# Kernel optimization log

Hardware: AMD Instinct MI355X
Metric: run time of the kernel (lower is better)

Reference implementation:

```python
import jax, jax.numpy as jnp
import numpy as np

WS = 7  # window size

def rel_pos_index(ws):
    coords = np.stack(np.meshgrid(np.arange(ws), np.arange(ws), indexing='ij'))  # [2,ws,ws]
    cf = coords.reshape(2, -1)                      # [2, N]
    rel = (cf[:, :, None] - cf[:, None, :]).transpose(1, 2, 0)  # [N,N,2]
    rel[:, :, 0] += ws - 1
    rel[:, :, 1] += ws - 1
    rel[:, :, 0] *= 2 * ws - 1
    return rel.sum(-1)                              # [N,N] int

REL_IDX = rel_pos_index(WS)

def setup_inputs() -> dict:
    key = jax.random.key(0)
    ks = jax.random.split(key, 7)
    B, nW, H, N, D = 32, 64, 6, WS * WS, 32
    C = H * D
    return {
        "x": jax.random.normal(ks[0], (B * nW, N, C), jnp.float32),
        "q_global": jax.random.normal(ks[1], (B, 1, H, N, D), jnp.float32),
        "w_qkv": jax.random.normal(ks[2], (2 * C, C), jnp.float32) * 0.02,
        "b_qkv": jax.random.normal(ks[3], (2 * C,), jnp.float32) * 0.02,
        "bias_table": jax.random.normal(ks[4], ((2 * WS - 1) ** 2, H), jnp.float32) * 0.02,
        "w_proj": jax.random.normal(ks[5], (C, C), jnp.float32) * 0.02,
        "b_proj": jax.random.normal(ks[6], (C,), jnp.float32) * 0.02,
    }

def reference(x, q_global, w_qkv, b_qkv, bias_table, w_proj, b_proj):
    B_, N, C = x.shape
    B, _, H, _, D = q_global.shape
    scale = D ** -0.5
    # K,V projection: [B_, N, 2C] -> two [B_, H, N, D]
    kv = x @ w_qkv.T + b_qkv
    k, v = jnp.split(kv, 2, axis=-1)
    k = k.reshape(B_, N, H, D).transpose(0, 2, 1, 3)
    v = v.reshape(B_, N, H, D).transpose(0, 2, 1, 3)
    # Global query repeated over windows per image
    rep = B_ // B
    q = jnp.broadcast_to(q_global, (B, rep, H, N, D)).reshape(B_, H, N, D) * scale
    attn = jnp.einsum('bhnd,bhmd->bhnm', q, k)  # [B_, H, N, N]
    bias = bias_table[REL_IDX.reshape(-1)].reshape(N, N, H).transpose(2, 0, 1)  # [H,N,N]
    attn = jax.nn.softmax(attn + bias[None], axis=-1)
    out = jnp.einsum('bhnm,bhmd->bhnd', attn, v).transpose(0, 2, 1, 3).reshape(B_, N, C)
    return out @ w_proj.T + b_proj
```

## Files before the change

kernel.cpp:

```cpp
#include <hip/hip_runtime.h>
#include <hip/hip_bf16.h>

typedef __attribute__((ext_vector_type(8))) short short8;
typedef __attribute__((ext_vector_type(4))) short short4v;
typedef __attribute__((ext_vector_type(4))) float f32x4;
typedef __attribute__((ext_vector_type(4))) unsigned int uint32x4;

#define MFMA16(A,B,C) __builtin_amdgcn_mfma_f32_16x16x32_bf16((A),(B),(C),0,0,0)

static __device__ __forceinline__ unsigned short f2bf(float f) {
  return __builtin_bit_cast(unsigned short, __float2bfloat16(f));
}

__global__ void prep_kernel(const float* __restrict__ qg,
                            const float* __restrict__ wqkv,
                            const float* __restrict__ wproj,
                            const float* __restrict__ btab,
                            unsigned short* __restrict__ wq_c,
                            unsigned short* __restrict__ wp_c,
                            unsigned short* __restrict__ q_bf,
                            float* __restrict__ bias_c)
{
  const int t = blockIdx.x * 256 + threadIdx.x;
  if (t < 32*6*64*32) {
    const int d = t & 31, n = (t >> 5) & 63;
    const int bh = t >> 11;
    const int h = bh % 6, b = bh / 6;
    float v = 0.f;
    if (n < 49) v = qg[((b * 6 + h) * 49 + n) * 32 + d] * 0.17677669529663687f;
    q_bf[t] = f2bf(v);
  }
  if (t < 8*3*6*64*8) {
    const int e = t & 7, l = (t >> 3) & 63;
    const int kb = (t >> 9) % 6, g = (t >> 9) / 6;
    const int ct = g % 3, wv = g / 3;
    const int j = wv * 48 + ct * 16 + (l & 15);
    const int c = kb * 32 + (l >> 4) * 8 + e;
    wq_c[t] = f2bf(wqkv[j * 192 + c]);
  }
  if (t < 2*6*6*64*8) {
    const int e = t & 7, l = (t >> 3) & 63;
    const int kb = (t >> 9) % 6, g = (t >> 9) / 6;
    const int ct = g % 6, cc = g / 6;
    const int cp = cc * 96 + ct * 16 + (l & 15);
    const int c = kb * 32 + (l >> 4) * 8 + e;
    wp_c[t] = f2bf(wproj[cp * 192 + c]);
  }
  if (t < 6*4*64*16) {
    const int i4 = t & 15;
    const int mt = i4 >> 2, r = i4 & 3;
    const int l = (t >> 4) & 63;
    const int nt = (t >> 10) & 3;
    const int h = t >> 12;
    const int m = (l >> 4) * 8 + (mt & 1) * 4 + r + (mt >> 1) * 32;
    const int n = nt * 16 + (l & 15);
    float v;
    if (m >= 49) v = -1e30f;
    else if (n >= 49) v = 0.f;
    else {
      const int ci = n / 7, cj = n % 7, mi = m / 7, mj = m % 7;
      const int idx = (ci - mi + 6) * 13 + (cj - mj + 6);
      v = btab[idx * 6 + h];
    }
    bias_c[t] = v;
  }
}

__global__ __launch_bounds__(512, 4)
void fused_win_attn(const float* __restrict__ x,
                    const float* __restrict__ b_qkv,
                    const float* __restrict__ b_proj,
                    const unsigned short* __restrict__ wq_c,
                    const unsigned short* __restrict__ wp_c,
                    const unsigned short* __restrict__ q_bf,
                    const float* __restrict__ bias_c,
                    float* __restrict__ out)
{
  extern __shared__ unsigned short lds[];
  unsigned short* x_lds  = lds;
  unsigned short* k_lds  = lds + 12800;
  unsigned short* vT_lds = lds + 26624;
  unsigned short* o_lds  = lds + 12800;

  const f32x4 ZERO4 = {0.f, 0.f, 0.f, 0.f};
  const int tid = threadIdx.x;
  const int wv = tid >> 6;
  const int l  = tid & 63;
  const int lr = l & 15;
  const int lq = l >> 4;
  const int w  = blockIdx.x;

  {
    const float* xw = x + (size_t)w * (49 * 192);
    for (int i = tid; i < 2352; i += 512) {
      const float4 v = *reinterpret_cast<const float4*>(xw + i * 4);
      const int e = i * 4;
      const int row = e / 192, col = e % 192;
      short4v pk;
      pk[0] = (short)f2bf(v.x); pk[1] = (short)f2bf(v.y);
      pk[2] = (short)f2bf(v.z); pk[3] = (short)f2bf(v.w);
      *reinterpret_cast<short4v*>(&x_lds[row * 200 + col]) = pk;
    }
    for (int i = tid; i < 720; i += 512) {
      const int e = i * 4;
      const int row = 49 + e / 192, col = e % 192;
      short4v z = {0, 0, 0, 0};
      *reinterpret_cast<short4v*>(&x_lds[row * 200 + col]) = z;
    }
  }
  __syncthreads();

  {
    short8 afr[4][6];
#pragma unroll
    for (int mt = 0; mt < 4; ++mt)
#pragma unroll
      for (int kb = 0; kb < 6; ++kb)
        afr[mt][kb] = *reinterpret_cast<const short8*>(
            &x_lds[(mt * 16 + lr) * 200 + kb * 32 + lq * 8]);

    for (int ct = 0; ct < 3; ++ct) {
      const int j = wv * 48 + ct * 16 + lr;
      short8 bfr[6];
#pragma unroll
      for (int kb = 0; kb < 6; ++kb)
        bfr[kb] = *reinterpret_cast<const short8*>(
            &wq_c[((((wv * 3) + ct) * 6 + kb) * 64 + l) * 8]);
      const float bq = b_qkv[j];
      f32x4 acc[4];
#pragma unroll
      for (int mt = 0; mt < 4; ++mt) acc[mt] = ZERO4;
#pragma unroll
      for (int kb = 0; kb < 6; ++kb)
#pragma unroll
        for (int mt = 0; mt < 4; ++mt)
          acc[mt] = MFMA16(afr[mt][kb], bfr[kb], acc[mt]);

      if (j < 192) {
        const int h = j >> 5, d = j & 31;
#pragma unroll
        for (int mt = 0; mt < 4; ++mt) {
          const int n0 = mt * 16 + lq * 4;
#pragma unroll
          for (int r = 0; r < 4; ++r)
            k_lds[h * 2304 + (n0 + r) * 36 + d] = f2bf(acc[mt][r] + bq);
        }
      } else {
        const int jj = j - 192, h = jj >> 5, d = jj & 31;
#pragma unroll
        for (int mt = 0; mt < 4; ++mt) {
          const int n0 = mt * 16 + lq * 4;
          short4v pk;
#pragma unroll
          for (int r = 0; r < 4; ++r) pk[r] = (short)f2bf(acc[mt][r] + bq);
          *reinterpret_cast<short4v*>(&vT_lds[h * 2176 + d * 68 + n0]) = pk;
        }
      }
    }
  }
  __syncthreads();

  const int nt = wv & 3;
  const int img = w >> 6;
  const int rowbase = (lr >> 2) * 8 + (lr & 3);
  f32x4 o_reg[3][2];
#pragma unroll
  for (int rd = 0; rd < 3; ++rd) {
    const int h = (wv >> 2) + 2 * rd;
    const short8 aq = *reinterpret_cast<const short8*>(
        &q_bf[((img * 6 + h) * 64 + nt * 16 + lr) * 32 + lq * 8]);
    f32x4 s[4];
#pragma unroll
    for (int mt = 0; mt < 4; ++mt) {
      const int row = rowbase + (mt & 1) * 4 + (mt >> 1) * 32;
      const unsigned short* kp = &k_lds[h * 2304 + row * 36 + lq * 8];
      const short4v k0 = *reinterpret_cast<const short4v*>(kp);
      const short4v k1 = *reinterpret_cast<const short4v*>(kp + 4);
      short8 bk;
      bk[0]=k0[0]; bk[1]=k0[1]; bk[2]=k0[2]; bk[3]=k0[3];
      bk[4]=k1[0]; bk[5]=k1[1]; bk[6]=k1[2]; bk[7]=k1[3];
      s[mt] = MFMA16(bk, aq, ZERO4);
    }
    const float* bc = bias_c + ((h * 4 + nt) * 64 + l) * 16;
    float lsum = 0.f;
    unsigned int pa_u[4][2];
#pragma unroll
    for (int mt = 0; mt < 4; ++mt) {
      const float4 b4 = *reinterpret_cast<const float4*>(bc + mt * 4);
      const float p0 = __expf(s[mt][0] + b4.x);
      const float p1 = __expf(s[mt][1] + b4.y);
      const float p2 = __expf(s[mt][2] + b4.z);
      const float p3 = __expf(s[mt][3] + b4.w);
      lsum += (p0 + p1) + (p2 + p3);
      pa_u[mt][0] = (unsigned int)f2bf(p0) | ((unsigned int)f2bf(p1) << 16);
      pa_u[mt][1] = (unsigned int)f2bf(p2) | ((unsigned int)f2bf(p3) << 16);
    }
    lsum += __shfl_xor(lsum, 16, 64);
    lsum += __shfl_xor(lsum, 32, 64);
    const float rs = 1.0f / lsum;
    float rinv[4];
#pragma unroll
    for (int r = 0; r < 4; ++r)
      rinv[r] = __shfl(rs, lq * 4 + r, 16);
    f32x4 o0 = ZERO4, o1 = ZERO4;
#pragma unroll
    for (int kb = 0; kb < 2; ++kb) {
      uint32x4 uu;
      uu[0] = pa_u[2*kb][0]; uu[1] = pa_u[2*kb][1];
      uu[2] = pa_u[2*kb+1][0]; uu[3] = pa_u[2*kb+1][1];
      const short8 pa = __builtin_bit_cast(short8, uu);
      const unsigned short* vp0 = &vT_lds[h * 2176 + lr * 68 + kb * 32 + lq * 8];
      const unsigned short* vp1 = &vT_lds[h * 2176 + (16 + lr) * 68 + kb * 32 + lq * 8];
      const short4v a0 = *reinterpret_cast<const short4v*>(vp0);
      const short4v a1 = *reinterpret_cast<const short4v*>(vp0 + 4);
      short8 bv0; bv0[0]=a0[0];bv0[1]=a0[1];bv0[2]=a0[2];bv0[3]=a0[3];
                  bv0[4]=a1[0];bv0[5]=a1[1];bv0[6]=a1[2];bv0[7]=a1[3];
      o0 = MFMA16(pa, bv0, o0);
      const short4v c0 = *reinterpret_cast<const short4v*>(vp1);
      const short4v c1 = *reinterpret_cast<const short4v*>(vp1 + 4);
      short8 bv1; bv1[0]=c0[0];bv1[1]=c0[1];bv1[2]=c0[2];bv1[3]=c0[3];
                  bv1[4]=c1[0];bv1[5]=c1[1];bv1[6]=c1[2];bv1[7]=c1[3];
      o1 = MFMA16(pa, bv1, o1);
    }
#pragma unroll
    for (int r = 0; r < 4; ++r) {
      o_reg[rd][0][r] = o0[r] * rinv[r];
      o_reg[rd][1][r] = o1[r] * rinv[r];
    }
  }
  __syncthreads();

#pragma unroll
  for (int rd = 0; rd < 3; ++rd) {
    const int h = (wv >> 2) + 2 * rd;
#pragma unroll
    for (int r = 0; r < 4; ++r) {
      const int n = nt * 16 + lq * 4 + r;
      o_lds[n * 200 + h * 32 + lr]      = f2bf(o_reg[rd][0][r]);
      o_lds[n * 200 + h * 32 + 16 + lr] = f2bf(o_reg[rd][1][r]);
    }
  }
  __syncthreads();

  {
    const int mt = wv & 3;
    const int cc = wv >> 2;
    short8 af[6];
#pragma unroll
    for (int kb = 0; kb < 6; ++kb)
      af[kb] = *reinterpret_cast<const short8*>(&o_lds[(mt * 16 + lr) * 200 + kb * 32 + lq * 8]);
    float* op = out + (size_t)w * 9408;
    for (int ct = 0; ct < 6; ++ct) {
      const int cp = cc * 96 + ct * 16 + lr;
      short8 bf[6];
#pragma unroll
      for (int kb = 0; kb < 6; ++kb)
        bf[kb] = *reinterpret_cast<const short8*>(
            &wp_c[(((cc * 6 + ct) * 6 + kb) * 64 + l) * 8]);
      f32x4 acc = ZERO4;
#pragma unroll
      for (int kb = 0; kb < 6; ++kb) acc = MFMA16(af[kb], bf[kb], acc);
      const float bb = b_proj[cp];
      const int n0 = mt * 16 + lq * 4;
#pragma unroll
      for (int r = 0; r < 4; ++r)
        if (n0 + r < 49) op[(n0 + r) * 192 + cp] = acc[r] + bb;
    }
  }
}

extern "C" void kernel_launch(void* const* d_in, const int* in_sizes, int n_in,
                              void* d_out, int out_size, void* d_ws, size_t ws_size,
                              hipStream_t stream) {
  const float* x     = (const float*)d_in[0];
  const float* qg    = (const float*)d_in[1];
  const float* wqkv  = (const float*)d_in[2];
  const float* bqkv  = (const float*)d_in[3];
  const float* btab  = (const float*)d_in[4];
  const float* wproj = (const float*)d_in[5];
  const float* bproj = (const float*)d_in[6];
  float* out = (float*)d_out;

  char* ws = (char*)d_ws;
  unsigned short* wq_c  = (unsigned short*)(ws);
  unsigned short* wp_c  = (unsigned short*)(ws + 147456);
  unsigned short* q_bf  = (unsigned short*)(ws + 221184);
  float* bias_c         = (float*)(ws + 1007616);

  hipLaunchKernelGGL(prep_kernel, dim3(1536), dim3(256), 0, stream,
                     qg, wqkv, wproj, btab, wq_c, wp_c, q_bf, bias_c);
  hipLaunchKernelGGL(fused_win_attn, dim3(2048), dim3(512), 79360, stream,
                     x, bqkv, bproj, wq_c, wp_c, q_bf, bias_c, out);
}
```

Measured before the change: 90.54 us.

## Alias K/V buffers over x tile in LDS to raise occupancy

Restructures the KV projection so every wave first accumulates all three column tiles over the K dimension, then synchronizes before writing K and V^T into LDS space that overlaps the x tile. Trimming K rows to 56 shrinks the LDS footprint from about 79KB to 50KB, and the launch bounds rise from 4 to 6 waves-per-EU, so more blocks can be resident per CU. The cost is an extra barrier, 48 live accumulator registers, and tighter register pressure, which could cause spills.

```diff
diff --git a/kernel.cpp b/kernel.cpp
--- a/kernel.cpp
+++ b/kernel.cpp
@@ -66,7 +66,7 @@
   }
 }
 
-__global__ __launch_bounds__(512, 4)
+__global__ __launch_bounds__(512, 6)
 void fused_win_attn(const float* __restrict__ x,
                     const float* __restrict__ b_qkv,
                     const float* __restrict__ b_proj,
@@ -78,9 +78,9 @@
 {
   extern __shared__ unsigned short lds[];
   unsigned short* x_lds  = lds;
-  unsigned short* k_lds  = lds + 12800;
-  unsigned short* vT_lds = lds + 26624;
-  unsigned short* o_lds  = lds + 12800;
+  unsigned short* k_lds  = lds;
+  unsigned short* vT_lds = lds + 12096;
+  unsigned short* o_lds  = lds;
 
   const f32x4 ZERO4 = {0.f, 0.f, 0.f, 0.f};
   const int tid = threadIdx.x;
@@ -110,51 +110,52 @@
   }
   __syncthreads();
 
-  {
-    short8 afr[4][6];
+  f32x4 acc[3][4];
+#pragma unroll
+  for (int ct = 0; ct < 3; ++ct)
+#pragma unroll
+    for (int mt = 0; mt < 4; ++mt) acc[ct][mt] = ZERO4;
+#pragma unroll
+  for (int kb = 0; kb < 6; ++kb) {
+    short8 afr[4];
 #pragma unroll
     for (int mt = 0; mt < 4; ++mt)
-#pragma unroll
-      for (int kb = 0; kb < 6; ++kb)
-        afr[mt][kb] = *reinterpret_cast<const short8*>(
-            &x_lds[(mt * 16 + lr) * 200 + kb * 32 + lq * 8]);
-
+      afr[mt] = *reinterpret_cast<const short8*>(
+          &x_lds[(mt * 16 + lr) * 200 + kb * 32 + lq * 8]);
+#pragma unroll
     for (int ct = 0; ct < 3; ++ct) {
-      const int j = wv * 48 + ct * 16 + lr;
-      short8 bfr[6];
-#pragma unroll
-      for (int kb = 0; kb < 6; ++kb)
-        bfr[kb] = *reinterpret_cast<const short8*>(
-            &wq_c[((((wv * 3) + ct) * 6 + kb) * 64 + l) * 8]);
-      const float bq = b_qkv[j];
-      f32x4 acc[4];
-#pragma unroll
-      for (int mt = 0; mt < 4; ++mt) acc[mt] = ZERO4;
-#pragma unroll
-      for (int kb = 0; kb < 6; ++kb)
-#pragma unroll
-        for (int mt = 0; mt < 4; ++mt)
-          acc[mt] = MFMA16(afr[mt][kb], bfr[kb], acc[mt]);
-
-      if (j < 192) {
-        const int h = j >> 5, d = j & 31;
-#pragma unroll
-        for (int mt = 0; mt < 4; ++mt) {
-          const int n0 = mt * 16 + lq * 4;
-#pragma unroll
-          for (int r = 0; r < 4; ++r)
-            k_lds[h * 2304 + (n0 + r) * 36 + d] = f2bf(acc[mt][r] + bq);
-        }
-      } else {
-        const int jj = j - 192, h = jj >> 5, d = jj & 31;
-#pragma unroll
-        for (int mt = 0; mt < 4; ++mt) {
-          const int n0 = mt * 16 + lq * 4;
-          short4v pk;
-#pragma unroll
-          for (int r = 0; r < 4; ++r) pk[r] = (short)f2bf(acc[mt][r] + bq);
-          *reinterpret_cast<short4v*>(&vT_lds[h * 2176 + d * 68 + n0]) = pk;
-        }
+      const short8 bfr = *reinterpret_cast<const short8*>(
+          &wq_c[((((wv * 3) + ct) * 6 + kb) * 64 + l) * 8]);
+#pragma unroll
+      for (int mt = 0; mt < 4; ++mt)
+        acc[ct][mt] = MFMA16(afr[mt], bfr, acc[ct][mt]);
+    }
+  }
+  __syncthreads();
+
+#pragma unroll
+  for (int ct = 0; ct < 3; ++ct) {
+    const int j = wv * 48 + ct * 16 + lr;
+    const float bq = b_qkv[j];
+    if (wv < 4) {
+      const int h = j >> 5, d = j & 31;
+#pragma unroll
+      for (int mt = 0; mt < 4; ++mt) {
+        const int n0 = mt * 16 + lq * 4;
+#pragma unroll
+        for (int r = 0; r < 4; ++r)
+          if (n0 + r < 56)
+            k_lds[h * 2016 + (n0 + r) * 36 + d] = f2bf(acc[ct][mt][r] + bq);
+      }
+    } else {
+      const int jj = j - 192, h = jj >> 5, d = jj & 31;
+#pragma unroll
+      for (int mt = 0; mt < 4; ++mt) {
+        const int n0 = mt * 16 + lq * 4;
+        short4v pk;
+#pragma unroll
+        for (int r = 0; r < 4; ++r) pk[r] = (short)f2bf(acc[ct][mt][r] + bq);
+        *reinterpret_cast<short4v*>(&vT_lds[h * 2176 + d * 68 + n0]) = pk;
       }
     }
   }
@@ -173,7 +174,7 @@
 #pragma unroll
     for (int mt = 0; mt < 4; ++mt) {
       const int row = rowbase + (mt & 1) * 4 + (mt >> 1) * 32;
-      const unsigned short* kp = &k_lds[h * 2304 + row * 36 + lq * 8];
+      const unsigned short* kp = &k_lds[h * 2016 + row * 36 + lq * 8];
       const short4v k0 = *reinterpret_cast<const short4v*>(kp);
       const short4v k1 = *reinterpret_cast<const short4v*>(kp + 4);
       short8 bk;
@@ -257,14 +258,14 @@
       for (int kb = 0; kb < 6; ++kb)
         bf[kb] = *reinterpret_cast<const short8*>(
             &wp_c[(((cc * 6 + ct) * 6 + kb) * 64 + l) * 8]);
-      f32x4 acc = ZERO4;
-#pragma unroll
-      for (int kb = 0; kb < 6; ++kb) acc = MFMA16(af[kb], bf[kb], acc);
+      f32x4 acc2 = ZERO4;
+#pragma unroll
+      for (int kb = 0; kb < 6; ++kb) acc2 = MFMA16(af[kb], bf[kb], acc2);
       const float bb = b_proj[cp];
       const int n0 = mt * 16 + lq * 4;
 #pragma unroll
       for (int r = 0; r < 4; ++r)
-        if (n0 + r < 49) op[(n0 + r) * 192 + cp] = acc[r] + bb;
+        if (n0 + r < 49) op[(n0 + r) * 192 + cp] = acc2[r] + bb;
     }
   }
 }
@@ -289,6 +290,6 @@
 
   hipLaunchKernelGGL(prep_kernel, dim3(1536), dim3(256), 0, stream,
                      qg, wqkv, wproj, btab, wq_c, wp_c, q_bf, bias_c);
-  hipLaunchKernelGGL(fused_win_attn, dim3(2048), dim3(512), 79360, stream,
+  hipLaunchKernelGGL(fused_win_attn, dim3(2048), dim3(512), 50304, stream,
                      x, bqkv, bproj, wq_c, wp_c, q_bf, bias_c, out);
 }
```

Result: no change. 90.33 us (-0.2%).
